# Kernel tuning notes

Hardware: AMD Instinct MI355X
Metric: run time of the kernel (lower is better)

The kernel has to match this reference:

```python
import jax, jax.numpy as jnp
import numpy as np

B, N, M, G, F = 8, 1000, 64, 50, 128


def setup_inputs() -> dict:
    key = jax.random.key(0)
    ks = jax.random.split(key, 9)
    s = 0.05
    return {
        "features": jax.random.normal(ks[0], (B, N, F), jnp.float32),
        "rbf_expansion": jax.random.uniform(ks[1], (B, N, M, G), jnp.float32),
        "neighbor_list": jax.random.randint(ks[2], (B, N, M), 0, N, jnp.int64),
        "W_init": jax.random.normal(ks[3], (F, F), jnp.float32) * s,
        "W1": jax.random.normal(ks[4], (G, F), jnp.float32) * s,
        "b1": jnp.zeros((F,), jnp.float32),
        "W2": jax.random.normal(ks[5], (F, F), jnp.float32) * s,
        "b2": jnp.zeros((F,), jnp.float32),
        "nbr_w": jax.random.normal(ks[6], (F,), jnp.float32) * s,
        "Wo1": jax.random.normal(ks[7], (F, F), jnp.float32) * s,
        "bo1": jnp.zeros((F,), jnp.float32),
        "Wo2": jax.random.normal(ks[8], (F, F), jnp.float32) * s,
        "bo2": jnp.zeros((F,), jnp.float32),
    }


def reference(features, rbf_expansion, neighbor_list, W_init, W1, b1, W2, b2,
              nbr_w, Wo1, bo1, Wo2, bo2):
    b, n, m = neighbor_list.shape
    # 1. atom-wise linear, no bias/activation: [B,N,F]
    init = features @ W_init
    # 2. CFConv: filter generator on RBF expansion -> [B,N,M,F]
    filt = jnp.tanh(rbf_expansion @ W1 + b1) @ W2 + b2
    # gather neighbor features: init[b, neighbor_list[b,n,m], :] -> [B,N,M,F]
    idx = neighbor_list.reshape(b, n * m, 1)
    nbr_feat = jnp.take_along_axis(init, idx, axis=1).reshape(b, n, m, -1)
    conv = nbr_feat * filt
    # attention over neighbors via learned vector nbr_w
    attn = jax.nn.softmax(jnp.einsum('bnmf,f->bnm', conv, nbr_w), axis=-1)
    agg = jnp.einsum('bnm,bnmf->bnf', attn, conv)
    # 3-4. output dense: linear+tanh, then linear
    out = jnp.tanh(agg @ Wo1 + bo1) @ Wo2 + bo2
    return out, attn
```

## Files before the change

### kernel.cpp

```cpp
#include <hip/hip_runtime.h>
#include <hip/hip_bf16.h>

typedef __attribute__((ext_vector_type(8))) short short8;
typedef __attribute__((ext_vector_type(4))) float f32x4;
typedef unsigned short u16;
typedef unsigned int u32;

#define NBATCH 8
#define NA 1000
#define MD 64
#define GD 50
#define FD 128
#define TOTAL (NBATCH * NA)

__device__ __forceinline__ u16 f2bf(float f) {
    u32 x = __float_as_uint(f);
    return (u16)((x + 0x7fffu + ((x >> 16) & 1u)) >> 16);
}
__device__ __forceinline__ float bf2f(u16 u) {
    return __uint_as_float(((u32)u) << 16);
}
__device__ __forceinline__ u32 pkbf(float x, float y) {
    __hip_bfloat162 h = __float22bfloat162_rn(float2{x, y});
    return *reinterpret_cast<u32*>(&h);
}
__device__ __forceinline__ float tanh_fast(float x) {
    float e = __expf(2.0f * x);
    return 1.0f - 2.0f * __builtin_amdgcn_rcpf(e + 1.0f);
}
__device__ __forceinline__ f32x4 mfma16(short8 a, short8 b, f32x4 c) {
    return __builtin_amdgcn_mfma_f32_16x16x32_bf16(a, b, c, 0, 0, 0);
}

__global__ void k0_prep(const float* __restrict__ W1, const float* __restrict__ W2,
                        const float* __restrict__ Wi, const float* __restrict__ Wo1,
                        const float* __restrict__ Wo2,
                        u16* __restrict__ W1T, u16* __restrict__ W2T,
                        u16* __restrict__ WiT, u16* __restrict__ Wo1T,
                        u16* __restrict__ Wo2T) {
    const int g0 = blockIdx.x * 256 + threadIdx.x;
    const int gstep = gridDim.x * 256;
    for (int i = g0; i < 128 * 72; i += gstep) {
        int n = i / 72, k = i - n * 72;
        int ks = (k < GD) ? k : 0;
        W1T[i] = (k < GD) ? f2bf(W1[ks * FD + n]) : (u16)0;
    }
    for (int i = g0; i < 2 * 128 * 72; i += gstep) {
        int p = i / 9216;
        int rem = i - p * 9216;
        int n = rem / 72, kk = rem - n * 72;
        bool valid = kk < 64;
        int k = p * 64 + (valid ? kk : 0);
        W2T[i]  = valid ? f2bf(W2[k * FD + n])  : (u16)0;
        WiT[i]  = valid ? f2bf(Wi[k * FD + n])  : (u16)0;
        Wo1T[i] = valid ? f2bf(Wo1[k * FD + n]) : (u16)0;
        Wo2T[i] = valid ? f2bf(Wo2[k * FD + n]) : (u16)0;
    }
}

__global__ __launch_bounds__(256, 3) void k1_init(const float* __restrict__ feat,
                                                  const u16* __restrict__ WiT,
                                                  u16* __restrict__ initB) {
    __shared__ alignas(16) char smem[53248];
    u16* sA = (u16*)smem;
    u16* sW = (u16*)(smem + 34816);
    const int tid = threadIdx.x, wid = tid >> 6, lane = tid & 63;
    const int quad = lane >> 4, col = lane & 15, rw = wid * 32;
    const int row0 = blockIdx.x * 128;

    for (int i = tid; i < 4096; i += 256) {
        int r = i >> 5, c = (i & 31) * 4;
        int gr = row0 + r;
        float4 v = {0.f, 0.f, 0.f, 0.f};
        if (gr < TOTAL) v = *(const float4*)&feat[(size_t)gr * FD + c];
        u32* p = (u32*)&sA[r * 136 + c];
        p[0] = pkbf(v.x, v.y);
        p[1] = pkbf(v.z, v.w);
    }
    for (int i = tid; i < 1152; i += 256) ((int4*)sW)[i] = ((const int4*)WiT)[i];
    __syncthreads();

    f32x4 acc[2][8];
    const f32x4 zf = {0.f, 0.f, 0.f, 0.f};
#pragma unroll
    for (int mt = 0; mt < 2; ++mt)
#pragma unroll
        for (int nt = 0; nt < 8; ++nt) acc[mt][nt] = zf;

    for (int half = 0; half < 2; ++half) {
        if (half) {
            __syncthreads();
            for (int i = tid; i < 1152; i += 256)
                ((int4*)sW)[i] = ((const int4*)(WiT + 9216))[i];
            __syncthreads();
        }
#pragma unroll
        for (int ks = 0; ks < 2; ++ks) {
            const int ka = half * 64 + ks * 32 + quad * 8;
            const int kb = ks * 32 + quad * 8;
            short8 a0 = *(const short8*)&sA[(rw + col) * 136 + ka];
            short8 a1 = *(const short8*)&sA[(rw + 16 + col) * 136 + ka];
#pragma unroll
            for (int nt = 0; nt < 8; ++nt) {
                short8 bfr = *(const short8*)&sW[(nt * 16 + col) * 72 + kb];
                acc[0][nt] = mfma16(a0, bfr, acc[0][nt]);
                acc[1][nt] = mfma16(a1, bfr, acc[1][nt]);
            }
        }
    }
#pragma unroll
    for (int mt = 0; mt < 2; ++mt)
#pragma unroll
        for (int nt = 0; nt < 8; ++nt)
#pragma unroll
            for (int r = 0; r < 4; ++r) {
                int row = rw + mt * 16 + quad * 4 + r;
                int gr = row0 + row;
                if (gr < TOTAL)
                    initB[(size_t)gr * FD + nt * 16 + col] = f2bf(acc[mt][nt][r]);
            }
}

__global__ __launch_bounds__(256, 3) void k2_main(
    const float* __restrict__ rbf, const int* __restrict__ nl,
    const u16* __restrict__ initB,
    const u16* __restrict__ W1T, const u16* __restrict__ W2T,
    const float* __restrict__ b1, const float* __restrict__ b2,
    const float* __restrict__ nbrw,
    float* __restrict__ aggOut, float* __restrict__ attnO) {
    __shared__ alignas(16) char smem[53760];
    u16* sA = (u16*)smem;
    u16* sB = (u16*)(smem + 34816);
    int* nlS = (int*)(smem + 53248);
    float* logitS = (float*)smem;
    float* attnS  = (float*)(smem + 512);
    float* aggS   = (float*)(smem + 1024);

    const int tid = threadIdx.x, wid = tid >> 6, lane = tid & 63;
    const int quad = lane >> 4, col = lane & 15, rw = wid * 32;
    const int blk = blockIdx.x;
    const int b = blk / 500;
    const int n0 = (blk - b * 500) * 2;
    const int atom0 = b * NA + n0;
    const size_t rbf_base = (size_t)atom0 * (MD * GD);

    if (tid < 128) nlS[tid] = nl[atom0 * MD + tid];
    for (int i = tid; i < 128 * 14; i += 256) {
        int r = i / 14;
        sA[r * 72 + 50 + (i - r * 14)] = 0;
    }
    for (int i = tid; i < 3200; i += 256) {
        int e = 2 * i;
        int r = e / 50, g = e - r * 50;
        float2 v = *(const float2*)&rbf[rbf_base + e];
        *(u32*)&sA[r * 72 + g] = pkbf(v.x, v.y);
    }
    for (int i = tid; i < 1152; i += 256) ((int4*)sB)[i] = ((const int4*)W1T)[i];
    __syncthreads();

    f32x4 acc[2][8];
    const f32x4 zf = {0.f, 0.f, 0.f, 0.f};
#pragma unroll
    for (int mt = 0; mt < 2; ++mt)
#pragma unroll
        for (int nt = 0; nt < 8; ++nt) acc[mt][nt] = zf;
#pragma unroll
    for (int ks = 0; ks < 2; ++ks) {
        const int ka = ks * 32 + quad * 8;
        short8 a0 = *(const short8*)&sA[(rw + col) * 72 + ka];
        short8 a1 = *(const short8*)&sA[(rw + 16 + col) * 72 + ka];
#pragma unroll
        for (int nt = 0; nt < 8; ++nt) {
            short8 bfr = *(const short8*)&sB[(nt * 16 + col) * 72 + ka];
            acc[0][nt] = mfma16(a0, bfr, acc[0][nt]);
            acc[1][nt] = mfma16(a1, bfr, acc[1][nt]);
        }
    }
    __syncthreads();

    float bias[8];
#pragma unroll
    for (int nt = 0; nt < 8; ++nt) bias[nt] = b1[nt * 16 + col];
#pragma unroll
    for (int mt = 0; mt < 2; ++mt)
#pragma unroll
        for (int nt = 0; nt < 8; ++nt)
#pragma unroll
            for (int r = 0; r < 4; ++r) {
                int row = rw + mt * 16 + quad * 4 + r;
                sA[row * 136 + nt * 16 + col] =
                    f2bf(tanh_fast(acc[mt][nt][r] + bias[nt]));
            }
    for (int i = tid; i < 1152; i += 256) ((int4*)sB)[i] = ((const int4*)W2T)[i];
    __syncthreads();

    f32x4 acc2[2][8];
#pragma unroll
    for (int mt = 0; mt < 2; ++mt)
#pragma unroll
        for (int nt = 0; nt < 8; ++nt) acc2[mt][nt] = zf;
    for (int half = 0; half < 2; ++half) {
        if (half) {
            __syncthreads();
            for (int i = tid; i < 1152; i += 256)
                ((int4*)sB)[i] = ((const int4*)(W2T + 9216))[i];
            __syncthreads();
        }
#pragma unroll
        for (int ks = 0; ks < 2; ++ks) {
            const int ka = half * 64 + ks * 32 + quad * 8;
            const int kb = ks * 32 + quad * 8;
            short8 a0 = *(const short8*)&sA[(rw + col) * 136 + ka];
            short8 a1 = *(const short8*)&sA[(rw + 16 + col) * 136 + ka];
#pragma unroll
            for (int nt = 0; nt < 8; ++nt) {
                short8 bfr = *(const short8*)&sB[(nt * 16 + col) * 72 + kb];
                acc2[0][nt] = mfma16(a0, bfr, acc2[0][nt]);
                acc2[1][nt] = mfma16(a1, bfr, acc2[1][nt]);
            }
        }
    }

    float wv[8];
#pragma unroll
    for (int nt = 0; nt < 8; ++nt) {
        bias[nt] = b2[nt * 16 + col];
        wv[nt] = nbrw[nt * 16 + col];
    }
    int rowoff[2][4];
#pragma unroll
    for (int mt = 0; mt < 2; ++mt)
#pragma unroll
        for (int r = 0; r < 4; ++r) {
            int rr = rw + mt * 16 + quad * 4 + r;
            rowoff[mt][r] = (b * NA + nlS[rr]) * FD;
        }
    float part[2][4] = {{0.f, 0.f, 0.f, 0.f}, {0.f, 0.f, 0.f, 0.f}};
#pragma unroll
    for (int mt = 0; mt < 2; ++mt)
#pragma unroll
        for (int nt = 0; nt < 8; ++nt)
#pragma unroll
            for (int r = 0; r < 4; ++r) {
                float nb = bf2f(initB[rowoff[mt][r] + nt * 16 + col]);
                float cv = nb * (acc2[mt][nt][r] + bias[nt]);
                acc2[mt][nt][r] = cv;
                part[mt][r] += cv * wv[nt];
            }
#pragma unroll
    for (int d = 1; d < 16; d <<= 1)
#pragma unroll
        for (int mt = 0; mt < 2; ++mt)
#pragma unroll
            for (int r = 0; r < 4; ++r)
                part[mt][r] += __shfl_xor(part[mt][r], d, 64);
    __syncthreads();
    if (col == 0) {
#pragma unroll
        for (int mt = 0; mt < 2; ++mt)
#pragma unroll
            for (int r = 0; r < 4; ++r)
                logitS[rw + mt * 16 + quad * 4 + r] = part[mt][r];
    }
    __syncthreads();

    if (wid < 2) {
        float x = logitS[wid * 64 + lane];
        float m = x;
#pragma unroll
        for (int d = 1; d < 64; d <<= 1) m = fmaxf(m, __shfl_xor(m, d, 64));
        float e = __expf(x - m);
        float s = e;
#pragma unroll
        for (int d = 1; d < 64; d <<= 1) s += __shfl_xor(s, d, 64);
        float a = e / s;
        attnS[wid * 64 + lane] = a;
        attnO[(size_t)(atom0 + wid) * MD + lane] = a;
    }
    __syncthreads();

    float aggp[8] = {0.f, 0.f, 0.f, 0.f, 0.f, 0.f, 0.f, 0.f};
#pragma unroll
    for (int mt = 0; mt < 2; ++mt)
#pragma unroll
        for (int r = 0; r < 4; ++r) {
            float a = attnS[rw + mt * 16 + quad * 4 + r];
#pragma unroll
            for (int nt = 0; nt < 8; ++nt) aggp[nt] += a * acc2[mt][nt][r];
        }
#pragma unroll
    for (int d = 16; d < 64; d <<= 1)
#pragma unroll
        for (int nt = 0; nt < 8; ++nt) aggp[nt] += __shfl_xor(aggp[nt], d, 64);
    if (quad == 0) {
#pragma unroll
        for (int nt = 0; nt < 8; ++nt) aggS[wid * 128 + nt * 16 + col] = aggp[nt];
    }
    __syncthreads();
    {
        int a = tid >> 7;
        int c = tid & 127;
        float v = aggS[(2 * a) * 128 + c] + aggS[(2 * a + 1) * 128 + c];
        aggOut[(size_t)(atom0 + a) * FD + c] = v;
    }
}

__global__ __launch_bounds__(256, 3) void k3_out(
    float* __restrict__ outp, const u16* __restrict__ Wo1T,
    const u16* __restrict__ Wo2T, const float* __restrict__ bo1,
    const float* __restrict__ bo2) {
    __shared__ alignas(16) char smem[53248];
    u16* sA = (u16*)smem;
    u16* sW = (u16*)(smem + 34816);
    const int tid = threadIdx.x, wid = tid >> 6, lane = tid & 63;
    const int quad = lane >> 4, col = lane & 15, rw = wid * 32;
    const int row0 = blockIdx.x * 128;

    for (int i = tid; i < 4096; i += 256) {
        int r = i >> 5, c = (i & 31) * 4;
        int gr = row0 + r;
        float4 v = {0.f, 0.f, 0.f, 0.f};
        if (gr < TOTAL) v = *(const float4*)&outp[(size_t)gr * FD + c];
        u32* p = (u32*)&sA[r * 136 + c];
        p[0] = pkbf(v.x, v.y);
        p[1] = pkbf(v.z, v.w);
    }
    for (int i = tid; i < 1152; i += 256) ((int4*)sW)[i] = ((const int4*)Wo1T)[i];
    __syncthreads();

    f32x4 acc[2][8];
    const f32x4 zf = {0.f, 0.f, 0.f, 0.f};
#pragma unroll
    for (int mt = 0; mt < 2; ++mt)
#pragma unroll
        for (int nt = 0; nt < 8; ++nt) acc[mt][nt] = zf;
    for (int half = 0; half < 2; ++half) {
        if (half) {
            __syncthreads();
            for (int i = tid; i < 1152; i += 256)
                ((int4*)sW)[i] = ((const int4*)(Wo1T + 9216))[i];
            __syncthreads();
        }
#pragma unroll
        for (int ks = 0; ks < 2; ++ks) {
            const int ka = half * 64 + ks * 32 + quad * 8;
            const int kb = ks * 32 + quad * 8;
            short8 a0 = *(const short8*)&sA[(rw + col) * 136 + ka];
            short8 a1 = *(const short8*)&sA[(rw + 16 + col) * 136 + ka];
#pragma unroll
            for (int nt = 0; nt < 8; ++nt) {
                short8 bfr = *(const short8*)&sW[(nt * 16 + col) * 72 + kb];
                acc[0][nt] = mfma16(a0, bfr, acc[0][nt]);
                acc[1][nt] = mfma16(a1, bfr, acc[1][nt]);
            }
        }
    }
    __syncthreads();

    float bias[8];
#pragma unroll
    for (int nt = 0; nt < 8; ++nt) bias[nt] = bo1[nt * 16 + col];
#pragma unroll
    for (int mt = 0; mt < 2; ++mt)
#pragma unroll
        for (int nt = 0; nt < 8; ++nt)
#pragma unroll
            for (int r = 0; r < 4; ++r) {
                int row = rw + mt * 16 + quad * 4 + r;
                sA[row * 136 + nt * 16 + col] =
                    f2bf(tanh_fast(acc[mt][nt][r] + bias[nt]));
            }
    for (int i = tid; i < 1152; i += 256) ((int4*)sW)[i] = ((const int4*)Wo2T)[i];
    __syncthreads();

    f32x4 acc2[2][8];
#pragma unroll
    for (int mt = 0; mt < 2; ++mt)
#pragma unroll
        for (int nt = 0; nt < 8; ++nt) acc2[mt][nt] = zf;
    for (int half = 0; half < 2; ++half) {
        if (half) {
            __syncthreads();
            for (int i = tid; i < 1152; i += 256)
                ((int4*)sW)[i] = ((const int4*)(Wo2T + 9216))[i];
            __syncthreads();
        }
#pragma unroll
        for (int ks = 0; ks < 2; ++ks) {
            const int ka = half * 64 + ks * 32 + quad * 8;
            const int kb = ks * 32 + quad * 8;
            short8 a0 = *(const short8*)&sA[(rw + col) * 136 + ka];
            short8 a1 = *(const short8*)&sA[(rw + 16 + col) * 136 + ka];
#pragma unroll
            for (int nt = 0; nt < 8; ++nt) {
                short8 bfr = *(const short8*)&sW[(nt * 16 + col) * 72 + kb];
                acc2[0][nt] = mfma16(a0, bfr, acc2[0][nt]);
                acc2[1][nt] = mfma16(a1, bfr, acc2[1][nt]);
            }
        }
    }
#pragma unroll
    for (int nt = 0; nt < 8; ++nt) bias[nt] = bo2[nt * 16 + col];
#pragma unroll
    for (int mt = 0; mt < 2; ++mt)
#pragma unroll
        for (int nt = 0; nt < 8; ++nt)
#pragma unroll
            for (int r = 0; r < 4; ++r) {
                int row = rw + mt * 16 + quad * 4 + r;
                int gr = row0 + row;
                if (gr < TOTAL)
                    outp[(size_t)gr * FD + nt * 16 + col] =
                        acc2[mt][nt][r] + bias[nt];
            }
}

extern "C" void kernel_launch(void* const* d_in, const int* in_sizes, int n_in,
                              void* d_out, int out_size, void* d_ws,
                              size_t ws_size, hipStream_t stream) {
    const float* feat = (const float*)d_in[0];
    const float* rbf  = (const float*)d_in[1];
    const int*   nl   = (const int*)d_in[2];
    const float* Wi   = (const float*)d_in[3];
    const float* W1   = (const float*)d_in[4];
    const float* b1   = (const float*)d_in[5];
    const float* W2   = (const float*)d_in[6];
    const float* b2   = (const float*)d_in[7];
    const float* nbrw = (const float*)d_in[8];
    const float* Wo1  = (const float*)d_in[9];
    const float* bo1  = (const float*)d_in[10];
    const float* Wo2  = (const float*)d_in[11];
    const float* bo2  = (const float*)d_in[12];

    float* outp  = (float*)d_out;
    float* attnp = outp + (size_t)TOTAL * FD;

    char* ws = (char*)d_ws;
    u16* initB = (u16*)ws;
    u16* W1T   = (u16*)(ws + 2048000);
    u16* W2T   = (u16*)(ws + 2048000 + 18432);
    u16* WiT   = (u16*)(ws + 2048000 + 18432 + 36864);
    u16* Wo1T  = (u16*)(ws + 2048000 + 18432 + 2 * 36864);
    u16* Wo2T  = (u16*)(ws + 2048000 + 18432 + 3 * 36864);

    hipLaunchKernelGGL(k0_prep, dim3(40), dim3(256), 0, stream,
                       W1, W2, Wi, Wo1, Wo2, W1T, W2T, WiT, Wo1T, Wo2T);
    hipLaunchKernelGGL(k1_init, dim3(63), dim3(256), 0, stream, feat, WiT, initB);
    hipLaunchKernelGGL(k2_main, dim3(4000), dim3(256), 0, stream,
                       rbf, nl, initB, W1T, W2T, b1, b2, nbrw, outp, attnp);
    hipLaunchKernelGGL(k3_out, dim3(63), dim3(256), 0, stream,
                       outp, Wo1T, Wo2T, bo1, bo2);
}
```

Before: 297.1 us.

## Split k2 waves by output columns and keep filter weights in registers

Wave tiling in the main CFConv kernel changes from row blocks (32 neighbor rows × all 128 features) to column blocks (all 128 rows × 32 features per wave). Each wave then loads its W1/W2 slices straight into registers, so the shared-memory weight staging and its extra barriers go away. LDS use falls enough to raise the occupancy hint from 3 to 4 blocks. In exchange, attention logits need a cross-wave partial sum through shared memory, and each wave reads all A rows from LDS.

```diff
diff --git a/kernel.cpp b/kernel.cpp
--- a/kernel.cpp
+++ b/kernel.cpp
@@ -121,29 +121,39 @@
             }
 }
 
-__global__ __launch_bounds__(256, 3) void k2_main(
+__global__ __launch_bounds__(256, 4) void k2_main(
     const float* __restrict__ rbf, const int* __restrict__ nl,
     const u16* __restrict__ initB,
     const u16* __restrict__ W1T, const u16* __restrict__ W2T,
     const float* __restrict__ b1, const float* __restrict__ b2,
     const float* __restrict__ nbrw,
     float* __restrict__ aggOut, float* __restrict__ attnO) {
-    __shared__ alignas(16) char smem[53760];
+    __shared__ alignas(16) char smem[37376];
     u16* sA = (u16*)smem;
-    u16* sB = (u16*)(smem + 34816);
-    int* nlS = (int*)(smem + 53248);
-    float* logitS = (float*)smem;
-    float* attnS  = (float*)(smem + 512);
-    float* aggS   = (float*)(smem + 1024);
+    int* nlS = (int*)(smem + 34816);
+    float* logitP = (float*)(smem + 35328);
+    float* attnS = (float*)smem;
 
     const int tid = threadIdx.x, wid = tid >> 6, lane = tid & 63;
-    const int quad = lane >> 4, col = lane & 15, rw = wid * 32;
+    const int quad = lane >> 4, col = lane & 15;
+    const int nt0 = 2 * wid;
     const int blk = blockIdx.x;
     const int b = blk / 500;
     const int n0 = (blk - b * 500) * 2;
     const int atom0 = b * NA + n0;
     const size_t rbf_base = (size_t)atom0 * (MD * GD);
 
+    short8 w1f[2][2];
+#pragma unroll
+    for (int n = 0; n < 2; ++n)
+#pragma unroll
+        for (int ks = 0; ks < 2; ++ks)
+            w1f[n][ks] = *(const short8*)&W1T[((nt0 + n) * 16 + col) * 72 +
+                                              ks * 32 + quad * 8];
+    float b1v[2];
+#pragma unroll
+    for (int n = 0; n < 2; ++n) b1v[n] = b1[(nt0 + n) * 16 + col];
+
     if (tid < 128) nlS[tid] = nl[atom0 * MD + tid];
     for (int i = tid; i < 128 * 14; i += 256) {
         int r = i / 14;
@@ -155,153 +165,128 @@
         float2 v = *(const float2*)&rbf[rbf_base + e];
         *(u32*)&sA[r * 72 + g] = pkbf(v.x, v.y);
     }
-    for (int i = tid; i < 1152; i += 256) ((int4*)sB)[i] = ((const int4*)W1T)[i];
-    __syncthreads();
-
-    f32x4 acc[2][8];
+    __syncthreads();
+
+    f32x4 acc1[8][2];
     const f32x4 zf = {0.f, 0.f, 0.f, 0.f};
 #pragma unroll
-    for (int mt = 0; mt < 2; ++mt)
-#pragma unroll
-        for (int nt = 0; nt < 8; ++nt) acc[mt][nt] = zf;
-#pragma unroll
-    for (int ks = 0; ks < 2; ++ks) {
-        const int ka = ks * 32 + quad * 8;
-        short8 a0 = *(const short8*)&sA[(rw + col) * 72 + ka];
-        short8 a1 = *(const short8*)&sA[(rw + 16 + col) * 72 + ka];
-#pragma unroll
-        for (int nt = 0; nt < 8; ++nt) {
-            short8 bfr = *(const short8*)&sB[(nt * 16 + col) * 72 + ka];
-            acc[0][nt] = mfma16(a0, bfr, acc[0][nt]);
-            acc[1][nt] = mfma16(a1, bfr, acc[1][nt]);
-        }
-    }
-    __syncthreads();
-
-    float bias[8];
-#pragma unroll
-    for (int nt = 0; nt < 8; ++nt) bias[nt] = b1[nt * 16 + col];
-#pragma unroll
-    for (int mt = 0; mt < 2; ++mt)
-#pragma unroll
-        for (int nt = 0; nt < 8; ++nt)
+    for (int m = 0; m < 8; ++m) {
+        acc1[m][0] = zf;
+        acc1[m][1] = zf;
+    }
+#pragma unroll
+    for (int ks = 0; ks < 2; ++ks)
+#pragma unroll
+        for (int m = 0; m < 8; ++m) {
+            short8 a = *(const short8*)&sA[(m * 16 + col) * 72 + ks * 32 + quad * 8];
+            acc1[m][0] = mfma16(a, w1f[0][ks], acc1[m][0]);
+            acc1[m][1] = mfma16(a, w1f[1][ks], acc1[m][1]);
+        }
+    __syncthreads();
+
+#pragma unroll
+    for (int m = 0; m < 8; ++m)
+#pragma unroll
+        for (int n = 0; n < 2; ++n)
 #pragma unroll
             for (int r = 0; r < 4; ++r) {
-                int row = rw + mt * 16 + quad * 4 + r;
-                sA[row * 136 + nt * 16 + col] =
-                    f2bf(tanh_fast(acc[mt][nt][r] + bias[nt]));
-            }
-    for (int i = tid; i < 1152; i += 256) ((int4*)sB)[i] = ((const int4*)W2T)[i];
-    __syncthreads();
-
-    f32x4 acc2[2][8];
-#pragma unroll
-    for (int mt = 0; mt < 2; ++mt)
-#pragma unroll
-        for (int nt = 0; nt < 8; ++nt) acc2[mt][nt] = zf;
-    for (int half = 0; half < 2; ++half) {
-        if (half) {
-            __syncthreads();
-            for (int i = tid; i < 1152; i += 256)
-                ((int4*)sB)[i] = ((const int4*)(W2T + 9216))[i];
-            __syncthreads();
-        }
-#pragma unroll
-        for (int ks = 0; ks < 2; ++ks) {
-            const int ka = half * 64 + ks * 32 + quad * 8;
-            const int kb = ks * 32 + quad * 8;
-            short8 a0 = *(const short8*)&sA[(rw + col) * 136 + ka];
-            short8 a1 = *(const short8*)&sA[(rw + 16 + col) * 136 + ka];
-#pragma unroll
-            for (int nt = 0; nt < 8; ++nt) {
-                short8 bfr = *(const short8*)&sB[(nt * 16 + col) * 72 + kb];
-                acc2[0][nt] = mfma16(a0, bfr, acc2[0][nt]);
-                acc2[1][nt] = mfma16(a1, bfr, acc2[1][nt]);
-            }
-        }
-    }
-
-    float wv[8];
-#pragma unroll
-    for (int nt = 0; nt < 8; ++nt) {
-        bias[nt] = b2[nt * 16 + col];
-        wv[nt] = nbrw[nt * 16 + col];
-    }
-    int rowoff[2][4];
-#pragma unroll
-    for (int mt = 0; mt < 2; ++mt)
+                int row = m * 16 + quad * 4 + r;
+                sA[row * 136 + (nt0 + n) * 16 + col] =
+                    f2bf(tanh_fast(acc1[m][n][r] + b1v[n]));
+            }
+    short8 w2f[2][4];
+#pragma unroll
+    for (int n = 0; n < 2; ++n)
+#pragma unroll
+        for (int kb = 0; kb < 4; ++kb)
+            w2f[n][kb] = *(const short8*)&W2T[(kb >> 1) * 9216 +
+                                              ((nt0 + n) * 16 + col) * 72 +
+                                              (kb & 1) * 32 + quad * 8];
+    float b2v[2], wvv[2];
+#pragma unroll
+    for (int n = 0; n < 2; ++n) {
+        b2v[n] = b2[(nt0 + n) * 16 + col];
+        wvv[n] = nbrw[(nt0 + n) * 16 + col];
+    }
+    __syncthreads();
+
+    f32x4 acc2[8][2];
+#pragma unroll
+    for (int m = 0; m < 8; ++m) {
+        acc2[m][0] = zf;
+        acc2[m][1] = zf;
+    }
+#pragma unroll
+    for (int kb = 0; kb < 4; ++kb)
+#pragma unroll
+        for (int m = 0; m < 8; ++m) {
+            short8 a = *(const short8*)&sA[(m * 16 + col) * 136 + kb * 32 + quad * 8];
+            acc2[m][0] = mfma16(a, w2f[0][kb], acc2[m][0]);
+            acc2[m][1] = mfma16(a, w2f[1][kb], acc2[m][1]);
+        }
+
+#pragma unroll
+    for (int m = 0; m < 8; ++m)
 #pragma unroll
         for (int r = 0; r < 4; ++r) {
-            int rr = rw + mt * 16 + quad * 4 + r;
-            rowoff[mt][r] = (b * NA + nlS[rr]) * FD;
-        }
-    float part[2][4] = {{0.f, 0.f, 0.f, 0.f}, {0.f, 0.f, 0.f, 0.f}};
-#pragma unroll
-    for (int mt = 0; mt < 2; ++mt)
-#pragma unroll
-        for (int nt = 0; nt < 8; ++nt)
-#pragma unroll
-            for (int r = 0; r < 4; ++r) {
-                float nb = bf2f(initB[rowoff[mt][r] + nt * 16 + col]);
-                float cv = nb * (acc2[mt][nt][r] + bias[nt]);
-                acc2[mt][nt][r] = cv;
-                part[mt][r] += cv * wv[nt];
-            }
-#pragma unroll
-    for (int d = 1; d < 16; d <<= 1)
-#pragma unroll
-        for (int mt = 0; mt < 2; ++mt)
-#pragma unroll
-            for (int r = 0; r < 4; ++r)
-                part[mt][r] += __shfl_xor(part[mt][r], d, 64);
-    __syncthreads();
-    if (col == 0) {
-#pragma unroll
-        for (int mt = 0; mt < 2; ++mt)
-#pragma unroll
-            for (int r = 0; r < 4; ++r)
-                logitS[rw + mt * 16 + quad * 4 + r] = part[mt][r];
-    }
+            int row = m * 16 + quad * 4 + r;
+            int ro = (b * NA + nlS[row]) * FD;
+            float p = 0.f;
+#pragma unroll
+            for (int n = 0; n < 2; ++n) {
+                float nb = bf2f(initB[ro + (nt0 + n) * 16 + col]);
+                float cv = (acc2[m][n][r] + b2v[n]) * nb;
+                acc2[m][n][r] = cv;
+                p += cv * wvv[n];
+            }
+#pragma unroll
+            for (int d = 1; d < 16; d <<= 1) p += __shfl_xor(p, d, 64);
+            if (col == 0) logitP[wid * 128 + row] = p;
+        }
     __syncthreads();
 
     if (wid < 2) {
-        float x = logitS[wid * 64 + lane];
-        float m = x;
-#pragma unroll
-        for (int d = 1; d < 64; d <<= 1) m = fmaxf(m, __shfl_xor(m, d, 64));
-        float e = __expf(x - m);
+        int row = wid * 64 + lane;
+        float x = logitP[row] + logitP[128 + row] + logitP[256 + row] +
+                  logitP[384 + row];
+        float mx = x;
+#pragma unroll
+        for (int d = 1; d < 64; d <<= 1) mx = fmaxf(mx, __shfl_xor(mx, d, 64));
+        float e = __expf(x - mx);
         float s = e;
 #pragma unroll
         for (int d = 1; d < 64; d <<= 1) s += __shfl_xor(s, d, 64);
         float a = e / s;
-        attnS[wid * 64 + lane] = a;
+        attnS[row] = a;
         attnO[(size_t)(atom0 + wid) * MD + lane] = a;
     }
     __syncthreads();
 
-    float aggp[8] = {0.f, 0.f, 0.f, 0.f, 0.f, 0.f, 0.f, 0.f};
-#pragma unroll
-    for (int mt = 0; mt < 2; ++mt)
+    float aggp[2][2] = {{0.f, 0.f}, {0.f, 0.f}};
+#pragma unroll
+    for (int m = 0; m < 8; ++m) {
+        int at = m >> 2;
 #pragma unroll
         for (int r = 0; r < 4; ++r) {
-            float a = attnS[rw + mt * 16 + quad * 4 + r];
-#pragma unroll
-            for (int nt = 0; nt < 8; ++nt) aggp[nt] += a * acc2[mt][nt][r];
-        }
+            float a = attnS[m * 16 + quad * 4 + r];
+            aggp[at][0] += a * acc2[m][0][r];
+            aggp[at][1] += a * acc2[m][1][r];
+        }
+    }
 #pragma unroll
     for (int d = 16; d < 64; d <<= 1)
 #pragma unroll
-        for (int nt = 0; nt < 8; ++nt) aggp[nt] += __shfl_xor(aggp[nt], d, 64);
+        for (int at = 0; at < 2; ++at) {
+            aggp[at][0] += __shfl_xor(aggp[at][0], d, 64);
+            aggp[at][1] += __shfl_xor(aggp[at][1], d, 64);
+        }
     if (quad == 0) {
 #pragma unroll
-        for (int nt = 0; nt < 8; ++nt) aggS[wid * 128 + nt * 16 + col] = aggp[nt];
-    }
-    __syncthreads();
-    {
-        int a = tid >> 7;
-        int c = tid & 127;
-        float v = aggS[(2 * a) * 128 + c] + aggS[(2 * a + 1) * 128 + c];
-        aggOut[(size_t)(atom0 + a) * FD + c] = v;
+        for (int at = 0; at < 2; ++at)
+#pragma unroll
+            for (int n = 0; n < 2; ++n)
+                aggOut[(size_t)(atom0 + at) * FD + (nt0 + n) * 16 + col] =
+                    aggp[at][n];
     }
 }
 
```

Result: no change. 301.9 us (+1.6%).
